# Kernel optimization log

Hardware: AMD Instinct MI355X
Metric: run time of the kernel (lower is better)

The kernel has to match this reference:

```python
import math
import jax, jax.numpy as jnp
import numpy as np

N_STEPS = 5
STEP = 0.1      # step_size buffer (eval mode: never updated)
LMBD = 0.1
MU = 0.0
N_DICT = 1


def _prox(c):
    # elasnet_prox: softshrink(c * s_mu, lmbd*step * s_mu); with mu=0, s_mu=1
    s_mu = 1.0 / (1.0 + MU * STEP)
    lam = LMBD * STEP * s_mu
    c = c * s_mu
    return jnp.sign(c) * jnp.maximum(jnp.abs(c) - lam, 0.0)


def _fista(x, W):
    # x: [N, C], W: [D, C]; F.linear(x, W) == x @ W.T
    s = STEP
    # i == 0
    c = jax.nn.relu(_prox(s * (x @ W.T)))
    # i == 1
    c_pre = c
    r = x - c @ W                      # residual [N, C]
    c = jax.nn.relu(_prox(c + s * (r @ W.T)))
    t = (math.sqrt(5.0) + 1.0) / 2.0
    # i >= 2: FISTA momentum, gradient evaluated at c (as in source)
    for _ in range(2, N_STEPS):
        t_pre = t
        t = (math.sqrt(1.0 + 4.0 * t_pre * t_pre) + 1.0) / 2.0
        a = (t_pre + t - 1.0) / t * c + (1.0 - t_pre) / t * c_pre
        c_pre = c
        r = x - c @ W
        c = jax.nn.relu(_prox(a + s * (r @ W.T)))
    return c


def setup_inputs() -> dict:
    key = jax.random.key(0)
    k1, k2 = jax.random.split(key)
    x = jax.random.normal(k1, (8, 2048, 512), dtype=jnp.float32)
    # kaiming-uniform-like dictionary [dict_size, n_channel]
    bound = math.sqrt(6.0 / 512.0)
    weight = jax.random.uniform(k2, (2048, 512), dtype=jnp.float32,
                                minval=-bound, maxval=bound)
    return {"x": x, "weight": weight}


def reference(x, weight):
    bs, tok, dim = x.shape
    xf = x.reshape(-1, dim)                    # [N, C]
    c = _fista(xf, weight)                     # [N, D]
    xp = c @ weight                            # [N, C]
    r = xf - xp
    r_loss = jnp.sum(r * r) / N_DICT
    c_loss = LMBD * jnp.sum(jnp.abs(c)) + 0.5 * MU * jnp.sum(c * c)
    return (c.reshape(bs, tok, -1), xp.reshape(bs, tok, -1), r, r_loss, c_loss)
```

## Files before the change

### kernel.cpp

```cpp
#include <hip/hip_runtime.h>
#include <cmath>


typedef __attribute__((ext_vector_type(8))) short bf16x8;
typedef __attribute__((ext_vector_type(8))) unsigned short u16x8;
typedef __attribute__((ext_vector_type(4))) float f32x4;

constexpr float S_STEP = 0.1f;
constexpr float LAM    = 0.01f;

__device__ __forceinline__ unsigned short f2bf(float f) {
    unsigned u = __float_as_uint(f);
    u += 0x7FFFu + ((u >> 16) & 1u);
    return (unsigned short)(u >> 16);
}
__device__ __forceinline__ float bf2f(unsigned short s) {
    return __uint_as_float(((unsigned)s) << 16);
}

__device__ __forceinline__ void async16(const void* g, void* l) {
    __builtin_amdgcn_global_load_lds(
        (const __attribute__((address_space(1))) void*)g,
        (__attribute__((address_space(3))) void*)l, 16, 0, 0);
}

template<int EPI>
__global__ __launch_bounds__(256)
void gemm_bt(const short* __restrict__ A, const short* __restrict__ B,
             int K, int Nn, int lbx,
             const unsigned short* Cc, const unsigned short* Cpre,
             const unsigned short* __restrict__ Xb, const float* __restrict__ Xf,
             unsigned short* OutB, float* Out32, float* R32,
             float cfA, float cfB, float* loss)
{
    __shared__ __align__(16) unsigned char smem[32768];
    short* S  = (short*)smem;
    float (*L)[132] = (float (*)[132])smem;
    float* red2 = (float*)(smem + 32736);

    const int tid  = threadIdx.x;
    const int wave = tid >> 6;
    const int lane = tid & 63;

    const int qchunk = gridDim.x >> 3;
    const int idx    = (blockIdx.x & 7) * qchunk + (blockIdx.x >> 3);
    const int rowBase = (idx >> lbx) * 128;
    const int colBase = (idx & ((1 << lbx) - 1)) * 128;

    const int sRow = lane >> 2;
    const int sK   = (lane & 3) << 3;
    const short* gA = A + (size_t)(rowBase + wave * 32 + sRow) * K + sK;
    const short* gB = B + (size_t)(colBase + wave * 32 + sRow) * K + sK;
    const size_t rstep = (size_t)16 * K;
    short* lA = S + (wave * 32) * 32;
    short* lB = S + 8192 + (wave * 32) * 32;

    const int m16  = lane & 15;
    const int quad = lane >> 4;
    const short* paBase = S + ((wave & 1) * 64 + m16) * 32 + quad * 8;
    const short* pbBase = S + 8192 + ((wave >> 1) * 64 + m16) * 32 + quad * 8;

    f32x4 acc[4][4] = {};
    const int nIter = K >> 5;

    {
        async16(gA,         lA);
        async16(gA + rstep, lA + 512);
        async16(gB,         lB);
        async16(gB + rstep, lB + 512);
    }

    for (int it = 0; it < nIter; ++it) {
        __syncthreads();
        if (it + 1 < nIter) {
            const int nb = (it + 1) & 1;
            const int kb = (it + 1) << 5;
            async16(gA + kb,         lA + nb * 4096);
            async16(gA + kb + rstep, lA + nb * 4096 + 512);
            async16(gB + kb,         lB + nb * 4096);
            async16(gB + kb + rstep, lB + nb * 4096 + 512);
        }
        const int cb = (it & 1) * 4096;
        bf16x8 af[4], bfr[4];
        #pragma unroll
        for (int i = 0; i < 4; ++i) af[i]  = *(const bf16x8*)(paBase + cb + i * 512);
        #pragma unroll
        for (int j = 0; j < 4; ++j) bfr[j] = *(const bf16x8*)(pbBase + cb + j * 512);
        #pragma unroll
        for (int i = 0; i < 4; ++i)
            #pragma unroll
            for (int j = 0; j < 4; ++j)
                acc[i][j] = __builtin_amdgcn_mfma_f32_16x16x32_bf16(
                                af[i], bfr[j], acc[i][j], 0, 0, 0);
    }

    const int lrow = tid >> 3;
    const int seg  = tid & 7;
    const bool useCp = (cfB != 0.f);
    float lsum = 0.f;

    auto gofs = [&](int t) -> size_t {
        return (size_t)(rowBase + t * 32 + lrow) * Nn + colBase + seg * 16;
    };

    u16x8 cc0{}, cc1{}, cp0{}, cp1{}, xq0{}, xq1{};
    float xfv[16];
    if constexpr (EPI == 1 || EPI == 2) {
        const size_t g = gofs(0);
        cc0 = *(const u16x8*)(Cc + g); cc1 = *(const u16x8*)(Cc + g + 8);
        if (useCp) { cp0 = *(const u16x8*)(Cpre + g); cp1 = *(const u16x8*)(Cpre + g + 8); }
    } else if constexpr (EPI == 3) {
        const size_t g = gofs(0);
        xq0 = *(const u16x8*)(Xb + g); xq1 = *(const u16x8*)(Xb + g + 8);
    } else if constexpr (EPI == 4) {
        const size_t g = gofs(0);
        #pragma unroll
        for (int q = 0; q < 4; ++q)
            *(f32x4*)&xfv[q * 4] = *(const f32x4*)(Xf + g + q * 4);
    }

    #pragma unroll
    for (int t = 0; t < 4; ++t) {
        __syncthreads();
        if ((wave & 1) == (t >> 1)) {
            #pragma unroll
            for (int ii = 0; ii < 2; ++ii) {
                const int i   = (t & 1) * 2 + ii;
                const int lr0 = ii * 16 + quad * 4;
                #pragma unroll
                for (int r = 0; r < 4; ++r)
                    #pragma unroll
                    for (int j = 0; j < 4; ++j)
                        L[lr0 + r][(wave >> 1) * 64 + j * 16 + m16] = acc[i][j][r];
            }
        }
        __syncthreads();

        float v[16];
        #pragma unroll
        for (int q = 0; q < 4; ++q)
            *(f32x4*)&v[q * 4] = *(const f32x4*)&L[lrow][seg * 16 + q * 4];

        const size_t gidx = gofs(t);

        u16x8 ncc0{}, ncc1{}, ncp0{}, ncp1{}, nxq0{}, nxq1{};
        float nxfv[16];
        if (t < 3) {
            const size_t gn = gofs(t + 1);
            if constexpr (EPI == 1 || EPI == 2) {
                ncc0 = *(const u16x8*)(Cc + gn); ncc1 = *(const u16x8*)(Cc + gn + 8);
                if (useCp) { ncp0 = *(const u16x8*)(Cpre + gn); ncp1 = *(const u16x8*)(Cpre + gn + 8); }
            } else if constexpr (EPI == 3) {
                nxq0 = *(const u16x8*)(Xb + gn); nxq1 = *(const u16x8*)(Xb + gn + 8);
            } else if constexpr (EPI == 4) {
                #pragma unroll
                for (int q = 0; q < 4; ++q)
                    *(f32x4*)&nxfv[q * 4] = *(const f32x4*)(Xf + gn + q * 4);
            }
        }

        if constexpr (EPI == 0) {
            u16x8 o0, o1;
            #pragma unroll
            for (int k = 0; k < 8; ++k) {
                o0[k] = f2bf(fmaxf(S_STEP * v[k]     - LAM, 0.f));
                o1[k] = f2bf(fmaxf(S_STEP * v[k + 8] - LAM, 0.f));
            }
            *(u16x8*)(OutB + gidx)     = o0;
            *(u16x8*)(OutB + gidx + 8) = o1;
        } else if constexpr (EPI == 1 || EPI == 2) {
            float w[16];
            #pragma unroll
            for (int k = 0; k < 8; ++k) {
                w[k]     = fmaxf(cfA * bf2f(cc0[k]) + cfB * bf2f(cp0[k])
                                 + S_STEP * v[k]     - LAM, 0.f);
                w[k + 8] = fmaxf(cfA * bf2f(cc1[k]) + cfB * bf2f(cp1[k])
                                 + S_STEP * v[k + 8] - LAM, 0.f);
            }
            u16x8 o0, o1;
            #pragma unroll
            for (int k = 0; k < 8; ++k) { o0[k] = f2bf(w[k]); o1[k] = f2bf(w[k + 8]); }
            *(u16x8*)(OutB + gidx)     = o0;
            *(u16x8*)(OutB + gidx + 8) = o1;
            if constexpr (EPI == 2) {
                #pragma unroll
                for (int q = 0; q < 4; ++q)
                    *(f32x4*)(Out32 + gidx + q * 4) = *(const f32x4*)&w[q * 4];
                #pragma unroll
                for (int k = 0; k < 16; ++k) lsum += w[k];
            }
        } else if constexpr (EPI == 3) {
            u16x8 o0, o1;
            #pragma unroll
            for (int k = 0; k < 8; ++k) {
                o0[k] = f2bf(bf2f(xq0[k]) - v[k]);
                o1[k] = f2bf(bf2f(xq1[k]) - v[k + 8]);
            }
            *(u16x8*)(OutB + gidx)     = o0;
            *(u16x8*)(OutB + gidx + 8) = o1;
        } else {
            float rv[16];
            #pragma unroll
            for (int k = 0; k < 16; ++k) {
                rv[k] = xfv[k] - v[k];
                lsum += rv[k] * rv[k];
            }
            #pragma unroll
            for (int q = 0; q < 4; ++q) {
                *(f32x4*)(Out32 + gidx + q * 4) = *(const f32x4*)&v[q * 4];
                *(f32x4*)(R32   + gidx + q * 4) = *(const f32x4*)&rv[q * 4];
            }
        }

        if (t < 3) {
            if constexpr (EPI == 1 || EPI == 2) {
                cc0 = ncc0; cc1 = ncc1;
                if (useCp) { cp0 = ncp0; cp1 = ncp1; }
            } else if constexpr (EPI == 3) {
                xq0 = nxq0; xq1 = nxq1;
            } else if constexpr (EPI == 4) {
                #pragma unroll
                for (int k = 0; k < 16; ++k) xfv[k] = nxfv[k];
            }
        }
    }

    if constexpr (EPI == 2 || EPI == 4) {
        #pragma unroll
        for (int off = 32; off; off >>= 1) lsum += __shfl_down(lsum, off, 64);
        if (lane == 0) red2[wave] = lsum;
        __syncthreads();
        if (tid == 0) {
            const float s = red2[0] + red2[1] + red2[2] + red2[3];
            atomicAdd(loss, (EPI == 2) ? 0.1f * s : s);
        }
    }
}

__global__ __launch_bounds__(256)
void cvt_w_k(const float* __restrict__ W,
             unsigned short* __restrict__ Wb, unsigned short* __restrict__ Wtb)
{
    __shared__ unsigned short T[64][65];
    const int dBase = blockIdx.y * 64;
    const int cBase = blockIdx.x * 64;
    const int lc = threadIdx.x & 63;
    const int lr = threadIdx.x >> 6;
    #pragma unroll
    for (int p = 0; p < 16; ++p) {
        const int dl = p * 4 + lr;
        const size_t idx = (size_t)(dBase + dl) * 512 + cBase + lc;
        const unsigned short b = f2bf(W[idx]);
        Wb[idx] = b;
        T[dl][lc] = b;
    }
    __syncthreads();
    #pragma unroll
    for (int p = 0; p < 16; ++p) {
        const int cl = p * 4 + lr;
        Wtb[(size_t)(cBase + cl) * 2048 + dBase + lc] = T[lc][cl];
    }
}

__global__ __launch_bounds__(256)
void cvt_x_k(const float4* __restrict__ x4, ushort4* __restrict__ xb4, int n4)
{
    for (int i = blockIdx.x * 256 + threadIdx.x; i < n4; i += gridDim.x * 256) {
        const float4 v = x4[i];
        xb4[i] = make_ushort4(f2bf(v.x), f2bf(v.y), f2bf(v.z), f2bf(v.w));
    }
}

__global__ __launch_bounds__(256)
void copy_wtb_k(const u16x8* __restrict__ src, u16x8* __restrict__ dst)
{
    const int i = blockIdx.x * 256 + threadIdx.x;
    dst[i] = src[i];
}

extern "C" void kernel_launch(void* const* d_in, const int* in_sizes, int n_in,
                              void* d_out, int out_size, void* d_ws, size_t ws_size,
                              hipStream_t stream)
{
    (void)in_sizes; (void)n_in; (void)out_size; (void)ws_size;

    constexpr int N = 16384, C = 512, D = 2048;
    constexpr size_t ND = (size_t)N * D;
    constexpr size_t NC = (size_t)N * C;

    const float* x = (const float*)d_in[0];
    const float* W = (const float*)d_in[1];

    float* out    = (float*)d_out;
    float* c_out  = out;
    float* xp_out = out + ND;
    float* r_out  = out + ND + NC;
    float* rloss  = out + ND + 2 * NC;
    float* closs  = rloss + 1;

    short* cb0 = (short*)d_ws;
    short* cb1 = cb0 + ND;

    unsigned short* rb  = (unsigned short*)xp_out;
    unsigned short* Wb  = (unsigned short*)xp_out + NC;
    unsigned short* Wtb = (unsigned short*)r_out;
    unsigned short* xb  = (unsigned short*)r_out + (size_t)D * C;

    hipMemsetAsync((void*)rloss, 0, 2 * sizeof(float), stream);

    double tp = (std::sqrt(5.0) + 1.0) / 2.0;
    float cfA[5] = {0.f, 1.f, 0.f, 0.f, 0.f};
    float cfB[5] = {0.f, 0.f, 0.f, 0.f, 0.f};
    for (int i = 2; i < 5; ++i) {
        double t = (std::sqrt(1.0 + 4.0 * tp * tp) + 1.0) / 2.0;
        cfA[i] = (float)((tp + t - 1.0) / t);
        cfB[i] = (float)((1.0 - tp) / t);
        tp = t;
    }

    const dim3 blk(256);
    cvt_w_k<<<dim3(C / 64, D / 64), blk, 0, stream>>>(W, Wb, Wtb);
    cvt_x_k<<<dim3(1024), blk, 0, stream>>>((const float4*)x, (ushort4*)xb,
                                            (int)(NC / 4));

    const dim3 gridD((D / 128) * (N / 128));
    const dim3 gridC((C / 128) * (N / 128));
    constexpr int LBX_D = 4, LBX_C = 2;

    gemm_bt<0><<<gridD, blk, 0, stream>>>((const short*)xb, (const short*)Wb,
                                          C, D, LBX_D, nullptr, nullptr,
                                          nullptr, nullptr,
                                          (unsigned short*)cb0, nullptr, nullptr,
                                          0.f, 0.f, nullptr);

    short* bufs[2] = {cb0, cb1};
    for (int i = 1; i < 5; ++i) {
        const short* cprev = bufs[(i - 1) & 1];
        short*       cnew  = bufs[i & 1];
        const unsigned short* cpre2 =
            (i == 1) ? (const unsigned short*)cprev : (const unsigned short*)cnew;
        gemm_bt<3><<<gridC, blk, 0, stream>>>(cprev, (const short*)Wtb,
                                              D, C, LBX_C, nullptr, nullptr,
                                              xb, nullptr,
                                              rb, nullptr, nullptr,
                                              0.f, 0.f, nullptr);
        if (i < 4)
            gemm_bt<1><<<gridD, blk, 0, stream>>>((const short*)rb, (const short*)Wb,
                                                  C, D, LBX_D,
                                                  (const unsigned short*)cprev,
                                                  cpre2, nullptr, nullptr,
                                                  (unsigned short*)cnew, nullptr,
                                                  nullptr, cfA[i], cfB[i], nullptr);
        else
            gemm_bt<2><<<gridD, blk, 0, stream>>>((const short*)rb, (const short*)Wb,
                                                  C, D, LBX_D,
                                                  (const unsigned short*)cprev,
                                                  cpre2, nullptr, nullptr,
                                                  (unsigned short*)cnew, c_out,
                                                  nullptr, cfA[i], cfB[i], closs);
    }

    copy_wtb_k<<<dim3(512), blk, 0, stream>>>((const u16x8*)Wtb, (u16x8*)cb1);

    gemm_bt<4><<<gridC, blk, 0, stream>>>(cb0, (const short*)cb1,
                                          D, C, LBX_C, nullptr, nullptr,
                                          nullptr, x,
                                          nullptr, xp_out, r_out,
                                          0.f, 0.f, rloss);
}
```

Baseline: 745.7 us.

## Triple-buffer GEMM K-loop with explicit vmcnt waits and one barrier

Moves the bf16 GEMM main loop from double to triple LDS buffering, issuing async global-to-LDS loads two K-steps ahead. The implicit waits of __syncthreads are replaced by explicit s_waitcnt vmcnt and s_barrier, so each iteration waits only for the stage it is about to read. The goal is to hide global load latency behind the MFMA work. Shared memory grows from 32 KB to 48 KB per block, which can lower occupancy.

```diff
diff --git a/kernel.cpp b/kernel.cpp
--- a/kernel.cpp
+++ b/kernel.cpp
@@ -33,10 +33,10 @@
              unsigned short* OutB, float* Out32, float* R32,
              float cfA, float cfB, float* loss)
 {
-    __shared__ __align__(16) unsigned char smem[32768];
+    __shared__ __align__(16) unsigned char smem[49152];
     short* S  = (short*)smem;
     float (*L)[132] = (float (*)[132])smem;
-    float* red2 = (float*)(smem + 32736);
+    float* red2 = (float*)(smem + 49088);
 
     const int tid  = threadIdx.x;
     const int wave = tid >> 6;
@@ -52,13 +52,13 @@
     const short* gA = A + (size_t)(rowBase + wave * 32 + sRow) * K + sK;
     const short* gB = B + (size_t)(colBase + wave * 32 + sRow) * K + sK;
     const size_t rstep = (size_t)16 * K;
-    short* lA = S + (wave * 32) * 32;
-    short* lB = S + 8192 + (wave * 32) * 32;
+    short* lA = S + wave * 1024;
+    short* lB = S + 4096 + wave * 1024;
 
     const int m16  = lane & 15;
     const int quad = lane >> 4;
     const short* paBase = S + ((wave & 1) * 64 + m16) * 32 + quad * 8;
-    const short* pbBase = S + 8192 + ((wave >> 1) * 64 + m16) * 32 + quad * 8;
+    const short* pbBase = S + 4096 + ((wave >> 1) * 64 + m16) * 32 + quad * 8;
 
     f32x4 acc[4][4] = {};
     const int nIter = K >> 5;
@@ -68,19 +68,31 @@
         async16(gA + rstep, lA + 512);
         async16(gB,         lB);
         async16(gB + rstep, lB + 512);
-    }
-
+        if (nIter > 1) {
+            async16(gA + 32,         lA + 8192);
+            async16(gA + 32 + rstep, lA + 8192 + 512);
+            async16(gB + 32,         lB + 8192);
+            async16(gB + 32 + rstep, lB + 8192 + 512);
+            asm volatile("s_waitcnt vmcnt(4)" ::: "memory");
+        } else {
+            asm volatile("s_waitcnt vmcnt(0)" ::: "memory");
+        }
+        __builtin_amdgcn_s_barrier();
+    }
+
+    int sSt = 2;
+    int sRd = 0;
     for (int it = 0; it < nIter; ++it) {
-        __syncthreads();
-        if (it + 1 < nIter) {
-            const int nb = (it + 1) & 1;
-            const int kb = (it + 1) << 5;
-            async16(gA + kb,         lA + nb * 4096);
-            async16(gA + kb + rstep, lA + nb * 4096 + 512);
-            async16(gB + kb,         lB + nb * 4096);
-            async16(gB + kb + rstep, lB + nb * 4096 + 512);
-        }
-        const int cb = (it & 1) * 4096;
+        if (it + 2 < nIter) {
+            const int kb = (it + 2) << 5;
+            short* sA = lA + sSt * 8192;
+            short* sB = lB + sSt * 8192;
+            async16(gA + kb,         sA);
+            async16(gA + kb + rstep, sA + 512);
+            async16(gB + kb,         sB);
+            async16(gB + kb + rstep, sB + 512);
+        }
+        const int cb = sRd * 8192;
         bf16x8 af[4], bfr[4];
         #pragma unroll
         for (int i = 0; i < 4; ++i) af[i]  = *(const bf16x8*)(paBase + cb + i * 512);
@@ -92,6 +104,11 @@
             for (int j = 0; j < 4; ++j)
                 acc[i][j] = __builtin_amdgcn_mfma_f32_16x16x32_bf16(
                                 af[i], bfr[j], acc[i][j], 0, 0, 0);
+        if (it + 2 < nIter)      asm volatile("s_waitcnt vmcnt(4)" ::: "memory");
+        else if (it + 1 < nIter) asm volatile("s_waitcnt vmcnt(0)" ::: "memory");
+        if (it + 1 < nIter) __builtin_amdgcn_s_barrier();
+        sSt = (sSt == 2) ? 0 : sSt + 1;
+        sRd = (sRd == 2) ? 0 : sRd + 1;
     }
 
     const int lrow = tid >> 3;
```

Result: faster. 718.3 us (-3.7%).
